# Kernel tuning notes

Hardware: AMD Instinct MI355X
Metric: run time of the kernel (lower is better)

## Reference

```python
import jax, jax.numpy as jnp
import numpy as np

D_MODEL = 2048
NUM_HEADS = 16
HEAD_DIM = 128
ROPE_BASE = 10000.0
NEG_INF = -1e9


def setup_inputs() -> dict:
    key = jax.random.key(0)
    ks = jax.random.split(key, 5)
    B, S = 2, 2048
    hidden_states = jax.random.normal(ks[0], (B, S, D_MODEL), dtype=jnp.float32)
    # additive causal mask: 0 on/below diagonal, large-negative above
    causal = jnp.triu(jnp.full((S, S), NEG_INF, dtype=jnp.float32), k=1)
    attention_mask = jnp.broadcast_to(causal, (B, 1, S, S))
    position_ids = jnp.broadcast_to(jnp.arange(S, dtype=jnp.int32), (B, S))
    scale = 1.0 / np.sqrt(D_MODEL)
    Wq = jax.random.normal(ks[1], (D_MODEL, NUM_HEADS * HEAD_DIM), dtype=jnp.float32) * scale
    Wk = jax.random.normal(ks[2], (D_MODEL, NUM_HEADS * HEAD_DIM), dtype=jnp.float32) * scale
    Wv = jax.random.normal(ks[3], (D_MODEL, NUM_HEADS * HEAD_DIM), dtype=jnp.float32) * scale
    Wo = jax.random.normal(ks[4], (NUM_HEADS * HEAD_DIM, D_MODEL), dtype=jnp.float32) * scale
    return {"hidden_states": hidden_states, "attention_mask": attention_mask,
            "position_ids": position_ids, "Wq": Wq, "Wk": Wk, "Wv": Wv, "Wo": Wo}


def _rope_cos_sin(position_ids):
    # inv_freq: [head_dim/2]
    inv_freq = 1.0 / (ROPE_BASE ** (jnp.arange(0, HEAD_DIM, 2, dtype=jnp.float32) / HEAD_DIM))
    freqs = position_ids.astype(jnp.float32)[..., None] * inv_freq  # [B,S,hd/2]
    emb = jnp.concatenate([freqs, freqs], axis=-1)  # [B,S,hd]
    return jnp.cos(emb), jnp.sin(emb)


def _rotate_half(x):
    x1, x2 = jnp.split(x, 2, axis=-1)
    return jnp.concatenate([-x2, x1], axis=-1)


def reference(hidden_states, attention_mask, position_ids, Wq, Wk, Wv, Wo):
    B, S, _ = hidden_states.shape
    H, Dh = NUM_HEADS, HEAD_DIM
    q = (hidden_states @ Wq).reshape(B, S, H, Dh).transpose(0, 2, 1, 3)  # [B,H,S,Dh]
    k = (hidden_states @ Wk).reshape(B, S, H, Dh).transpose(0, 2, 1, 3)
    v = (hidden_states @ Wv).reshape(B, S, H, Dh).transpose(0, 2, 1, 3)
    cos, sin = _rope_cos_sin(position_ids)  # [B,S,Dh]
    cos = cos[:, None, :, :]  # [B,1,S,Dh]
    sin = sin[:, None, :, :]
    q = q * cos + _rotate_half(q) * sin
    k = k * cos + _rotate_half(k) * sin
    scaling = 1.0 / np.sqrt(Dh)
    scores = jnp.einsum('bhqd,bhkd->bhqk', q, k) * scaling  # [B,H,S,S]
    scores = scores + attention_mask[:, :, :, :S]
    attn = jax.nn.softmax(scores.astype(jnp.float32), axis=-1).astype(q.dtype)
    # dropout p=0.0 / eval mode -> identity
    out = jnp.einsum('bhqk,bhkd->bhqd', attn, v)  # [B,H,S,Dh]
    out = out.transpose(0, 2, 1, 3).reshape(B, S, H * Dh)
    return out @ Wo
```

## Files before the change

### kernel.cpp

```cpp
#include <hip/hip_runtime.h>

typedef __attribute__((ext_vector_type(4))) float f32x4;
typedef __attribute__((ext_vector_type(8))) _Float16 f16x8;
typedef __attribute__((ext_vector_type(4))) _Float16 f16x4;

#define SEQ 2048
#define DM 2048
#define NQKV 6144

__device__ __forceinline__ void gload16(const _Float16* g, _Float16* l) {
  __builtin_amdgcn_global_load_lds(
      (const __attribute__((address_space(1))) void*)g,
      (__attribute__((address_space(3))) void*)l, 16, 0, 0);
}

__global__ __launch_bounds__(256) void cvt_x_kernel(const float* __restrict__ X,
                                                    _Float16* __restrict__ Xb, int n4) {
  int i = blockIdx.x * 256 + threadIdx.x;
  if (i < n4) {
    const float4 v = ((const float4*)X)[i];
    f16x4 o;
    o.x = (_Float16)v.x; o.y = (_Float16)v.y; o.z = (_Float16)v.z; o.w = (_Float16)v.w;
    ((f16x4*)Xb)[i] = o;
  }
}

__global__ __launch_bounds__(256) void wtrans_all_kernel(const float* __restrict__ Wq,
                                                         const float* __restrict__ Wk,
                                                         const float* __restrict__ Wv,
                                                         const float* __restrict__ Wo,
                                                         _Float16* __restrict__ Wqkvt,
                                                         _Float16* __restrict__ Wot) {
  __shared__ float tile[32][33];
  const int z = blockIdx.z;
  const float* W = (z == 0) ? Wq : (z == 1) ? Wk : (z == 2) ? Wv : Wo;
  _Float16* Wt = (z < 3) ? (Wqkvt + (size_t)z * 2048 * 2048) : Wot;
  const int n0 = blockIdx.x * 32, k0 = blockIdx.y * 32;
  const int tx = threadIdx.x & 31, ty = threadIdx.x >> 5;
#pragma unroll
  for (int i = 0; i < 32; i += 8)
    tile[ty + i][tx] = W[(size_t)(k0 + ty + i) * 2048 + n0 + tx];
  __syncthreads();
#pragma unroll
  for (int i = 0; i < 32; i += 8)
    Wt[(size_t)(n0 + ty + i) * 2048 + k0 + tx] = (_Float16)tile[tx][ty + i];
}

__global__ __launch_bounds__(256) void rope_table_kernel(float* __restrict__ ct,
                                                         float* __restrict__ st) {
  int i = blockIdx.x * 256 + threadIdx.x;
  int pos = i >> 6, f = i & 63;
  float inv = powf(10000.0f, -(float)f / 64.0f);
  float ang = (float)pos * inv;
  ct[i] = cosf(ang);
  st[i] = sinf(ang);
}

template <bool OUTF32>
__global__ __launch_bounds__(512, 2) void gemm8n_kernel(const _Float16* __restrict__ A,
                                                        const _Float16* __restrict__ Bt,
                                                        void* __restrict__ Cout,
                                                        int M, int N, int K) {
  __shared__ __align__(16) _Float16 As[2 * 16384];
  __shared__ __align__(16) _Float16 Bs[2 * 8192];
  const int nwg = gridDim.x * gridDim.y;
  const int orig = blockIdx.y * gridDim.x + blockIdx.x;
  const int id = (orig & 7) * (nwg >> 3) + (orig >> 3);
  const int bx = id % gridDim.x, by = id / gridDim.x;
  const int bm = by * 256, bn = bx * 128;
  const int t = threadIdx.x, lane = t & 63, w = t >> 6;
  const int wm = w >> 2, wn = w & 3;
  const int rl = lane & 15, lr4 = lane >> 4;
  const int NKT = K >> 6;

  const int srow = t >> 3;
  const int scol = ((t & 7) ^ (srow & 7)) << 3;
  const _Float16* pA = A + (size_t)(bm + srow) * K + scol;
  const _Float16* pB = Bt + (size_t)(bn + srow) * K + scol;
  _Float16* lA = As + t * 8;
  _Float16* lB = Bs + t * 8;
  const size_t rowK64 = (size_t)64 * K;

#define STA(H, KT, BUF)                                                    \
  { const size_t _g = (size_t)((H) * 128) * K + (size_t)(KT) * 64;         \
    gload16(pA + _g, lA + (BUF) * 16384 + (H) * 8192);                     \
    gload16(pA + _g + rowK64, lA + (BUF) * 16384 + (H) * 8192 + 4096); }
#define STB(KT, BUF)                                                       \
  { const size_t _g = (size_t)(KT) * 64;                                   \
    gload16(pB + _g, lB + (BUF) * 8192);                                   \
    gload16(pB + _g + rowK64, lB + (BUF) * 8192 + 4096); }

  const int sw0 = (lr4 ^ (rl & 7)) << 3;
  const int sw1 = ((4 + lr4) ^ (rl & 7)) << 3;
  const int aoff = (wm * 64 + rl) * 64;
  const int boff = (wn * 32 + rl) * 64;

  f16x8 a_[4][2], b_[2][2];
  f32x4 acc[2][4][2];
#pragma unroll
  for (int qm = 0; qm < 2; ++qm)
#pragma unroll
    for (int mf = 0; mf < 4; ++mf)
#pragma unroll
      for (int nf = 0; nf < 2; ++nf) acc[qm][mf][nf] = (f32x4)0.0f;

#define LOAD_A(H, BUF)                                                  \
  { const _Float16* _p = As + (BUF) * 16384 + (H) * 8192 + aoff;        \
    _Pragma("unroll") for (int mf = 0; mf < 4; ++mf) {                  \
      a_[mf][0] = *(const f16x8*)&_p[mf * 1024 + sw0];                  \
      a_[mf][1] = *(const f16x8*)&_p[mf * 1024 + sw1]; } }
#define LOAD_B(BUF)                                                     \
  { const _Float16* _p = Bs + (BUF) * 8192 + boff;                      \
    _Pragma("unroll") for (int nf = 0; nf < 2; ++nf) {                  \
      b_[nf][0] = *(const f16x8*)&_p[nf * 1024 + sw0];                  \
      b_[nf][1] = *(const f16x8*)&_p[nf * 1024 + sw1]; } }
#define MFMA_Q(QM)                                                      \
  __builtin_amdgcn_s_setprio(1);                                        \
  _Pragma("unroll") for (int mf = 0; mf < 4; ++mf)                      \
    _Pragma("unroll") for (int nf = 0; nf < 2; ++nf) {                  \
      acc[QM][mf][nf] = __builtin_amdgcn_mfma_f32_16x16x32_f16(         \
          a_[mf][0], b_[nf][0], acc[QM][mf][nf], 0, 0, 0);              \
      acc[QM][mf][nf] = __builtin_amdgcn_mfma_f32_16x16x32_f16(         \
          a_[mf][1], b_[nf][1], acc[QM][mf][nf], 0, 0, 0); }            \
  __builtin_amdgcn_s_setprio(0);
#define BAR()                                                           \
  do { __builtin_amdgcn_sched_barrier(0); __builtin_amdgcn_s_barrier(); \
       __builtin_amdgcn_sched_barrier(0); } while (0)
#define LGKM0()                                                         \
  do { asm volatile("s_waitcnt lgkmcnt(0)" ::: "memory");               \
       __builtin_amdgcn_sched_barrier(0); } while (0)

  STA(0, 0, 0); STB(0, 0); STA(1, 0, 0);
  STA(0, 1, 1); STB(1, 1);
  asm volatile("s_waitcnt vmcnt(4)" ::: "memory");
  BAR();

  for (int i = 0; i < (NKT >> 1) - 1; ++i) {
    const int j = 2 * i;
    LOAD_A(0, 0); LOAD_B(0); STA(1, j + 1, 1);
    BAR(); LGKM0(); MFMA_Q(0); BAR();
    LOAD_A(1, 0); STA(0, j + 2, 0); STB(j + 2, 0);
    asm volatile("s_waitcnt vmcnt(4)" ::: "memory");
    BAR(); LGKM0(); MFMA_Q(1); BAR();
    LOAD_A(0, 1); LOAD_B(1); STA(1, j + 2, 0);
    BAR(); LGKM0(); MFMA_Q(0); BAR();
    LOAD_A(1, 1); STA(0, j + 3, 1); STB(j + 3, 1);
    asm volatile("s_waitcnt vmcnt(4)" ::: "memory");
    BAR(); LGKM0(); MFMA_Q(1); BAR();
  }
  {
    LOAD_A(0, 0); LOAD_B(0); STA(1, NKT - 1, 1);
    BAR(); LGKM0(); MFMA_Q(0); BAR();
    LOAD_A(1, 0);
    asm volatile("s_waitcnt vmcnt(0)" ::: "memory");
    BAR(); LGKM0(); MFMA_Q(1); BAR();
    LOAD_A(0, 1); LOAD_B(1);
    BAR(); LGKM0(); MFMA_Q(0); BAR();
    LOAD_A(1, 1);
    BAR(); LGKM0(); MFMA_Q(1);
  }

#pragma unroll
  for (int qm = 0; qm < 2; ++qm)
#pragma unroll
    for (int mf = 0; mf < 4; ++mf)
#pragma unroll
      for (int nf = 0; nf < 2; ++nf) {
        const int col = bn + wn * 32 + nf * 16 + rl;
#pragma unroll
        for (int ri = 0; ri < 4; ++ri) {
          const int row = bm + qm * 128 + wm * 64 + mf * 16 + lr4 * 4 + ri;
          if (OUTF32)
            ((float*)Cout)[(size_t)row * N + col] = acc[qm][mf][nf][ri];
          else
            ((_Float16*)Cout)[(size_t)row * N + col] = (_Float16)acc[qm][mf][nf][ri];
        }
      }
#undef STA
#undef STB
#undef LOAD_A
#undef LOAD_B
#undef MFMA_Q
#undef BAR
#undef LGKM0
}

__global__ __launch_bounds__(256) void rope_qk_kernel(const _Float16* __restrict__ QKVo,
                                                      const int* __restrict__ pos_ids,
                                                      const float* __restrict__ ct,
                                                      const float* __restrict__ st,
                                                      _Float16* __restrict__ Q,
                                                      _Float16* __restrict__ K) {
  int id = blockIdx.x * 256 + threadIdx.x;
  int f = id & 63;
  int h = (id >> 6) & 15;
  int s_ = (id >> 10) & 2047;
  int b = (id >> 21) & 1;
  int row = b * SEQ + s_;
  int pos = pos_ids[row];
  float c = ct[pos * 64 + f], sn = st[pos * 64 + f];
  size_t base = (size_t)row * NQKV;
  float q1 = (float)QKVo[base + h * 128 + f];
  float q2 = (float)QKVo[base + h * 128 + f + 64];
  float k1 = (float)QKVo[base + 2048 + h * 128 + f];
  float k2 = (float)QKVo[base + 2048 + h * 128 + f + 64];
  const float scale = 0.08838834764831845f;
  size_t obase = (((size_t)(b * 16 + h)) * SEQ + s_) * 128;
  Q[obase + f]      = (_Float16)((q1 * c - q2 * sn) * scale);
  Q[obase + f + 64] = (_Float16)((q2 * c + q1 * sn) * scale);
  K[obase + f]      = (_Float16)(k1 * c - k2 * sn);
  K[obase + f + 64] = (_Float16)(k2 * c + k1 * sn);
}

__global__ __launch_bounds__(256) void v_transpose_kernel(const _Float16* __restrict__ QKVo,
                                                          _Float16* __restrict__ Vt) {
  __shared__ _Float16 tile[32][40];
  const int s0 = blockIdx.x * 32, d0 = blockIdx.y * 32, bh = blockIdx.z;
  const int b = bh >> 4, h = bh & 15;
  const int tx = threadIdx.x & 31, ty = threadIdx.x >> 5;
#pragma unroll
  for (int i = 0; i < 32; i += 8) {
    int s_ = s0 + ty + i;
    tile[ty + i][tx] = QKVo[(size_t)(b * SEQ + s_) * NQKV + 4096 + h * 128 + d0 + tx];
  }
  __syncthreads();
#pragma unroll
  for (int i = 0; i < 32; i += 8) {
    int d = d0 + ty + i;
    Vt[((size_t)bh * 128 + d) * SEQ + s0 + tx] = tile[tx][ty + i];
  }
}

__global__ __launch_bounds__(512) void attn_kernel(const _Float16* __restrict__ Q,
                                                   const _Float16* __restrict__ K,
                                                   const _Float16* __restrict__ Vt,
                                                   _Float16* __restrict__ O) {
  __shared__ __align__(16) _Float16 Ks[2][64 * 128];
  __shared__ __align__(16) _Float16 Vs[2][128 * 64];
  __shared__ __align__(16) _Float16 Ps[8][16 * 72];
  const int bh = blockIdx.x;
  const int pair = blockIdx.y;
  const int b = bh >> 4, h = bh & 15;
  const int t = threadIdx.x, lane = t & 63, w = t >> 6;
  const int lr = lane >> 4, lc = lane & 15;
  const _Float16* Qb = Q + (size_t)bh * SEQ * 128;
  const _Float16* Kb = K + (size_t)bh * SEQ * 128;
  const _Float16* Vb = Vt + (size_t)bh * 128 * SEQ;

  auto stage = [&](int buf, int kb) {
    const int k0 = kb * 64;
#pragma unroll
    for (int i = 0; i < 2; ++i) {
      const int c = i * 512 + t;
      const int row = c >> 4, u = c & 15;
      gload16(&Kb[(size_t)(k0 + row) * 128 + ((u ^ (row & 7)) * 8)], &Ks[buf][c * 8]);
    }
#pragma unroll
    for (int i = 0; i < 2; ++i) {
      const int c = i * 512 + t;
      const int dim = c >> 3, u = c & 7;
      gload16(&Vb[(size_t)dim * SEQ + k0 + ((u ^ (dim & 7)) * 8)], &Vs[buf][c * 8]);
    }
  };

  for (int half = 0; half < 2; ++half) {
    const int j = half ? (15 - pair) : pair;
    const int q0 = j * 128;
    const int nkb = 2 * j + 2;
    const int rowmin = q0 + w * 16;

    f16x8 qf[4];
    {
      const int qrow = q0 + w * 16 + lc;
#pragma unroll
      for (int kk = 0; kk < 4; ++kk)
        qf[kk] = *(const f16x8*)&Qb[(size_t)qrow * 128 + kk * 32 + lr * 8];
    }
    f32x4 acco[8];
#pragma unroll
    for (int i = 0; i < 8; ++i) acco[i] = (f32x4)0.0f;
    float m_r[4] = {-1e30f, -1e30f, -1e30f, -1e30f};
    float l_r[4] = {0.f, 0.f, 0.f, 0.f};

    stage(0, 0);
    __syncthreads();
    for (int kb = 0; kb < nkb; ++kb) {
      const int cur = kb & 1;
      if (kb + 1 < nkb) stage(cur ^ 1, kb + 1);
      const int k0 = kb * 64;
      if (k0 <= rowmin + 15) {
        f32x4 sacc[4];
#pragma unroll
        for (int jj = 0; jj < 4; ++jj) sacc[jj] = (f32x4)0.0f;
#pragma unroll
        for (int jj = 0; jj < 4; ++jj) {
          const int krow = jj * 16 + lc;
#pragma unroll
          for (int kk = 0; kk < 4; ++kk) {
            const int idx = (krow * 128 + kk * 32 + lr * 8) ^ ((krow & 7) << 3);
            f16x8 kf = *(const f16x8*)&Ks[cur][idx];
            sacc[jj] = __builtin_amdgcn_mfma_f32_16x16x32_f16(qf[kk], kf, sacc[jj], 0, 0, 0);
          }
        }
        const bool diag = (k0 + 63 > rowmin);
#pragma unroll
        for (int r = 0; r < 4; ++r) {
          const int rowi = rowmin + lr * 4 + r;
          float s[4], mx = -1e30f;
#pragma unroll
          for (int jj = 0; jj < 4; ++jj) {
            float sv = sacc[jj][r];
            if (diag && (k0 + jj * 16 + lc > rowi)) sv = -1e30f;
            s[jj] = sv;
            mx = fmaxf(mx, sv);
          }
#pragma unroll
          for (int msk = 1; msk < 16; msk <<= 1) mx = fmaxf(mx, __shfl_xor(mx, msk));
          const float mn = fmaxf(m_r[r], mx);
          const float sc = __expf(m_r[r] - mn);
          float rs = 0.f;
#pragma unroll
          for (int jj = 0; jj < 4; ++jj) {
            float pv = __expf(s[jj] - mn);
            rs += pv;
            Ps[w][(lr * 4 + r) * 72 + jj * 16 + lc] = (_Float16)pv;
          }
#pragma unroll
          for (int msk = 1; msk < 16; msk <<= 1) rs += __shfl_xor(rs, msk);
          l_r[r] = l_r[r] * sc + rs;
          m_r[r] = mn;
#pragma unroll
          for (int tt = 0; tt < 8; ++tt) acco[tt][r] *= sc;
        }
#pragma unroll
        for (int tt = 0; tt < 8; ++tt) {
          const int dim = tt * 16 + lc;
#pragma unroll
          for (int ch = 0; ch < 2; ++ch) {
            f16x8 pf = *(const f16x8*)&Ps[w][lc * 72 + ch * 32 + lr * 8];
            const int vidx = (dim * 64 + ch * 32 + lr * 8) ^ ((dim & 7) << 3);
            f16x8 vf = *(const f16x8*)&Vs[cur][vidx];
            acco[tt] = __builtin_amdgcn_mfma_f32_16x16x32_f16(pf, vf, acco[tt], 0, 0, 0);
          }
        }
      }
      __syncthreads();
    }
#pragma unroll
    for (int tt = 0; tt < 8; ++tt) {
      const int col = h * 128 + tt * 16 + lc;
#pragma unroll
      for (int r = 0; r < 4; ++r) {
        const int row = q0 + w * 16 + lr * 4 + r;
        O[(size_t)(b * SEQ + row) * DM + col] = (_Float16)(acco[tt][r] / l_r[r]);
      }
    }
  }
}

extern "C" void kernel_launch(void* const* d_in, const int* in_sizes, int n_in,
                              void* d_out, int out_size, void* d_ws, size_t ws_size,
                              hipStream_t stream) {
  const float* hidden = (const float*)d_in[0];
  const int* pos_ids = (const int*)d_in[2];
  const float* Wq = (const float*)d_in[3];
  const float* Wk = (const float*)d_in[4];
  const float* Wv = (const float*)d_in[5];
  const float* Wo = (const float*)d_in[6];

  char* ws = (char*)d_ws;
  _Float16* Xb    = (_Float16*)(ws + 0);
  _Float16* Wqkvt = (_Float16*)(ws + 16777216);
  _Float16* Wot   = (_Float16*)(ws + 41943040);
  _Float16* QKVo  = (_Float16*)(ws + 50331648);
  _Float16* Kbuf  = (_Float16*)(ws + 100663296);
  float* ct       = (float*)(ws + 117440512);
  float* st       = (float*)(ws + 117964800);
  _Float16* Vtbuf = Xb;
  _Float16* Qbuf  = Wqkvt;
  _Float16* Obuf  = QKVo;

  cvt_x_kernel<<<8192, 256, 0, stream>>>(hidden, Xb, 2097152);
  wtrans_all_kernel<<<dim3(64, 64, 4), 256, 0, stream>>>(Wq, Wk, Wv, Wo, Wqkvt, Wot);
  rope_table_kernel<<<512, 256, 0, stream>>>(ct, st);

  gemm8n_kernel<false><<<dim3(48, 16), 512, 0, stream>>>(Xb, Wqkvt, QKVo, 4096, 6144, 2048);

  rope_qk_kernel<<<16384, 256, 0, stream>>>(QKVo, pos_ids, ct, st, Qbuf, Kbuf);
  v_transpose_kernel<<<dim3(64, 4, 32), 256, 0, stream>>>(QKVo, Vtbuf);

  attn_kernel<<<dim3(32, 8), 512, 0, stream>>>(Qbuf, Kbuf, Vtbuf, Obuf);

  gemm8n_kernel<true><<<dim3(16, 16), 512, 0, stream>>>(Obuf, Wot, d_out, 4096, 2048, 2048);
}
```

Baseline: 303.6 us.

## Triple-buffer LDS tiles in the fp16 GEMM to deepen prefetch

Grows the shared-memory A/B staging from two to three k-tile slots and rewrites the main loop to process three k-tiles per iteration. Loads now run two tiles ahead, and the wait allows six outstanding global-to-LDS loads instead of four. The aim is to hide more global memory latency behind the MFMA work. In exchange, LDS use per block rises to about 144KB. The loop also now assumes (NKT-2) is divisible by 3, which holds for K=2048.

```diff
diff --git a/kernel.cpp b/kernel.cpp
--- a/kernel.cpp
+++ b/kernel.cpp
@@ -61,8 +61,8 @@
                                                         const _Float16* __restrict__ Bt,
                                                         void* __restrict__ Cout,
                                                         int M, int N, int K) {
-  __shared__ __align__(16) _Float16 As[2 * 16384];
-  __shared__ __align__(16) _Float16 Bs[2 * 8192];
+  __shared__ __align__(16) _Float16 As[3 * 16384];
+  __shared__ __align__(16) _Float16 Bs[3 * 8192];
   const int nwg = gridDim.x * gridDim.y;
   const int orig = blockIdx.y * gridDim.x + blockIdx.x;
   const int id = (orig & 7) * (nwg >> 3) + (orig >> 3);
@@ -81,14 +81,14 @@
   _Float16* lB = Bs + t * 8;
   const size_t rowK64 = (size_t)64 * K;
 
-#define STA(H, KT, BUF)                                                    \
+#define STA(H, KT, SLOT)                                                   \
   { const size_t _g = (size_t)((H) * 128) * K + (size_t)(KT) * 64;         \
-    gload16(pA + _g, lA + (BUF) * 16384 + (H) * 8192);                     \
-    gload16(pA + _g + rowK64, lA + (BUF) * 16384 + (H) * 8192 + 4096); }
-#define STB(KT, BUF)                                                       \
+    gload16(pA + _g, lA + (SLOT) * 16384 + (H) * 8192);                    \
+    gload16(pA + _g + rowK64, lA + (SLOT) * 16384 + (H) * 8192 + 4096); }
+#define STB(KT, SLOT)                                                      \
   { const size_t _g = (size_t)(KT) * 64;                                   \
-    gload16(pB + _g, lB + (BUF) * 8192);                                   \
-    gload16(pB + _g + rowK64, lB + (BUF) * 8192 + 4096); }
+    gload16(pB + _g, lB + (SLOT) * 8192);                                  \
+    gload16(pB + _g + rowK64, lB + (SLOT) * 8192 + 4096); }
 
   const int sw0 = (lr4 ^ (rl & 7)) << 3;
   const int sw1 = ((4 + lr4) ^ (rl & 7)) << 3;
@@ -104,13 +104,13 @@
 #pragma unroll
       for (int nf = 0; nf < 2; ++nf) acc[qm][mf][nf] = (f32x4)0.0f;
 
-#define LOAD_A(H, BUF)                                                  \
-  { const _Float16* _p = As + (BUF) * 16384 + (H) * 8192 + aoff;        \
+#define LOAD_A(H, SLOT)                                                 \
+  { const _Float16* _p = As + (SLOT) * 16384 + (H) * 8192 + aoff;       \
     _Pragma("unroll") for (int mf = 0; mf < 4; ++mf) {                  \
       a_[mf][0] = *(const f16x8*)&_p[mf * 1024 + sw0];                  \
       a_[mf][1] = *(const f16x8*)&_p[mf * 1024 + sw1]; } }
-#define LOAD_B(BUF)                                                     \
-  { const _Float16* _p = Bs + (BUF) * 8192 + boff;                      \
+#define LOAD_B(SLOT)                                                    \
+  { const _Float16* _p = Bs + (SLOT) * 8192 + boff;                     \
     _Pragma("unroll") for (int nf = 0; nf < 2; ++nf) {                  \
       b_[nf][0] = *(const f16x8*)&_p[nf * 1024 + sw0];                  \
       b_[nf][1] = *(const f16x8*)&_p[nf * 1024 + sw1]; } }
@@ -129,30 +129,33 @@
 #define LGKM0()                                                         \
   do { asm volatile("s_waitcnt lgkmcnt(0)" ::: "memory");               \
        __builtin_amdgcn_sched_barrier(0); } while (0)
+#define VM6() asm volatile("s_waitcnt vmcnt(6)" ::: "memory")
+#define VM0() asm volatile("s_waitcnt vmcnt(0)" ::: "memory")
 
   STA(0, 0, 0); STB(0, 0); STA(1, 0, 0);
-  STA(0, 1, 1); STB(1, 1);
-  asm volatile("s_waitcnt vmcnt(4)" ::: "memory");
+  STA(0, 1, 1); STB(1, 1); STA(1, 1, 1);
+  VM6();
   BAR();
 
-  for (int i = 0; i < (NKT >> 1) - 1; ++i) {
-    const int j = 2 * i;
-    LOAD_A(0, 0); LOAD_B(0); STA(1, j + 1, 1);
+  for (int jb = 0; jb + 4 < NKT; jb += 3) {
+    LOAD_A(0, 0); LOAD_B(0); STA(0, jb + 2, 2); STB(jb + 2, 2);
     BAR(); LGKM0(); MFMA_Q(0); BAR();
-    LOAD_A(1, 0); STA(0, j + 2, 0); STB(j + 2, 0);
-    asm volatile("s_waitcnt vmcnt(4)" ::: "memory");
-    BAR(); LGKM0(); MFMA_Q(1); BAR();
-    LOAD_A(0, 1); LOAD_B(1); STA(1, j + 2, 0);
+    LOAD_A(1, 0); STA(1, jb + 2, 2);
+    VM6(); BAR(); LGKM0(); MFMA_Q(1); BAR();
+    LOAD_A(0, 1); LOAD_B(1); STA(0, jb + 3, 0); STB(jb + 3, 0);
     BAR(); LGKM0(); MFMA_Q(0); BAR();
-    LOAD_A(1, 1); STA(0, j + 3, 1); STB(j + 3, 1);
-    asm volatile("s_waitcnt vmcnt(4)" ::: "memory");
-    BAR(); LGKM0(); MFMA_Q(1); BAR();
+    LOAD_A(1, 1); STA(1, jb + 3, 0);
+    VM6(); BAR(); LGKM0(); MFMA_Q(1); BAR();
+    LOAD_A(0, 2); LOAD_B(2); STA(0, jb + 4, 1); STB(jb + 4, 1);
+    BAR(); LGKM0(); MFMA_Q(0); BAR();
+    LOAD_A(1, 2); STA(1, jb + 4, 1);
+    VM6(); BAR(); LGKM0(); MFMA_Q(1); BAR();
   }
   {
-    LOAD_A(0, 0); LOAD_B(0); STA(1, NKT - 1, 1);
+    LOAD_A(0, 0); LOAD_B(0);
     BAR(); LGKM0(); MFMA_Q(0); BAR();
     LOAD_A(1, 0);
-    asm volatile("s_waitcnt vmcnt(0)" ::: "memory");
+    VM0();
     BAR(); LGKM0(); MFMA_Q(1); BAR();
     LOAD_A(0, 1); LOAD_B(1);
     BAR(); LGKM0(); MFMA_Q(0); BAR();
@@ -183,6 +186,8 @@
 #undef MFMA_Q
 #undef BAR
 #undef LGKM0
+#undef VM6
+#undef VM0
 }
 
 __global__ __launch_bounds__(256) void rope_qk_kernel(const _Float16* __restrict__ QKVo,
```

After: 296.0 us. 2.5% less time.
